# Kernel optimization log

Hardware: AMD Instinct MI355X
Metric: run time of the kernel (lower is better)

## Reference

```python
import jax, jax.numpy as jnp
import numpy as np

TOTAL_WORDS = 10000
EMBED_LEN = 100
SEQ_LEN = 80
BATCH = 2048
UNITS = 1024


def setup_inputs() -> dict:
    key = jax.random.key(0)
    ks = jax.random.split(key, 8)
    inputs = jax.random.randint(ks[0], (BATCH, SEQ_LEN), 0, TOTAL_WORDS)
    s = 0.02
    emb = jax.random.normal(ks[1], (TOTAL_WORDS, EMBED_LEN), jnp.float32) * s
    W0 = jax.random.normal(ks[2], (EMBED_LEN, 4 * UNITS), jnp.float32) * s
    U0 = jax.random.normal(ks[3], (UNITS, 4 * UNITS), jnp.float32) * s
    b0 = jnp.zeros((4 * UNITS,), jnp.float32)
    W1 = jax.random.normal(ks[4], (UNITS, 4 * UNITS), jnp.float32) * s
    U1 = jax.random.normal(ks[5], (UNITS, 4 * UNITS), jnp.float32) * s
    b1 = jnp.zeros((4 * UNITS,), jnp.float32)
    fcW = jax.random.normal(ks[6], (UNITS, 1), jnp.float32) * s
    fcb = jnp.zeros((1,), jnp.float32)
    return {"inputs": inputs, "emb": emb, "W0": W0, "U0": U0, "b0": b0,
            "W1": W1, "U1": U1, "b1": b1, "fcW": fcW, "fcb": fcb}


def _lstm_step(x, h, c, W, U, b):
    # Keras LSTMCell gate order: i, f, g(candidate), o
    z = x @ W + h @ U + b  # [B, 4*units]
    i, f, g, o = jnp.split(z, 4, axis=-1)
    i = jax.nn.sigmoid(i)
    f = jax.nn.sigmoid(f)
    g = jnp.tanh(g)
    o = jax.nn.sigmoid(o)
    c_new = f * c + i * g
    h_new = o * jnp.tanh(c_new)
    return h_new, c_new


def reference(inputs, emb, W0, U0, b0, W1, U1, b1, fcW, fcb):
    x = emb[inputs]                      # [B, T, E]
    xs = jnp.transpose(x, (1, 0, 2))     # [T, B, E] for scan over time
    B = inputs.shape[0]
    U = U0.shape[0]
    init = (jnp.zeros((B, U), x.dtype), jnp.zeros((B, U), x.dtype),
            jnp.zeros((B, U), x.dtype), jnp.zeros((B, U), x.dtype))

    def step(carry, xt):
        h0, c0, h1, c1 = carry
        h0, c0 = _lstm_step(xt, h0, c0, W0, U0, b0)
        h1, c1 = _lstm_step(h0, h1, c1, W1, U1, b1)
        return (h0, c0, h1, c1), None

    (h0, c0, h1, c1), _ = jax.lax.scan(step, init, xs)
    logits = h1 @ fcW + fcb              # [B, 1]
    return jax.nn.sigmoid(logits)
```

## Files before the change

### kernel.cpp

```cpp
#include <hip/hip_runtime.h>

#define DEVI __device__ __forceinline__

typedef __attribute__((ext_vector_type(4))) float f4;
typedef long long i64t;

DEVI unsigned char f2fp8(float x) {
  int p = __builtin_amdgcn_cvt_pk_fp8_f32(x, x, 0, false);
  return (unsigned char)(p & 0xff);
}
DEVI float fp82f(unsigned char b) {
  return __builtin_amdgcn_cvt_f32_fp8((int)b, 0);
}
DEVI float sigmoidf_(float x) { return 1.f / (1.f + __expf(-x)); }
DEVI float tanhf_(float x) {
  float ax = fabsf(x);
  float e = __expf(-2.f * ax);
  float t = (1.f - e) / (1.f + e);
  return x < 0.f ? -t : t;
}

#define GLDS16(g, l) __builtin_amdgcn_global_load_lds( \
    (const __attribute__((address_space(1))) void*)(g), \
    (__attribute__((address_space(3))) void*)(l), 16, 0, 0)

#define SCALE_UP 64.0f
#define SCALE_DN (1.0f / 4096.0f)


__global__ void k_conv_emb(const float* __restrict__ emb, unsigned char* __restrict__ ep) {
  int i = blockIdx.x * 256 + threadIdx.x;
  if (i >= 10000 * 128) return;
  int r = i >> 7, c = i & 127;
  ep[i] = (c < 100) ? f2fp8(emb[r * 100 + c] * SCALE_UP) : (unsigned char)0;
}

DEVI int permn(int n) {
  int g = n >> 10, u = n & 1023;
  return (u >> 5) * 128 + ((u >> 4) & 1) * 64 + g * 16 + (u & 15);
}
DEVI int kswz(int klog, int row) {
  return (klog & ~63) | (((((klog >> 3) & 7) ^ ((row >> 1) & 7))) << 3) | (klog & 7);
}

__global__ void k_conv_w0(const float* __restrict__ W0, const float* __restrict__ U0,
                          unsigned char* __restrict__ WT) {
  int i = blockIdx.x * 256 + threadIdx.x;
  if (i >= 4096 * 1152) return;
  int n = i / 1152, k = i - n * 1152;
  float v;
  if (k < 100) v = W0[k * 4096 + n];
  else if (k < 128) v = 0.f;
  else v = U0[(k - 128) * 4096 + n];
  int np = permn(n);
  WT[(size_t)np * 1152 + kswz(k, np)] = f2fp8(v * SCALE_UP);
}

__global__ void k_conv_w1(const float* __restrict__ W1, const float* __restrict__ U1,
                          unsigned char* __restrict__ WT) {
  int i = blockIdx.x * 256 + threadIdx.x;
  if (i >= 4096 * 2048) return;
  int n = i >> 11, k = i & 2047;
  float v = (k < 1024) ? W1[k * 4096 + n] : U1[(k - 1024) * 4096 + n];
  int np = permn(n);
  WT[(size_t)np * 2048 + kswz(k, np)] = f2fp8(v * SCALE_UP);
}


template<int K1, int KTOT, bool GATHER>
DEVI void lstm_body(int tile, char* smem,
    const unsigned char* __restrict__ src1,
    const unsigned char* __restrict__ src2,
    const int* __restrict__ idx, int t,
    const unsigned char* __restrict__ WT,
    const float* __restrict__ bias,
    float* __restrict__ cbuf,
    unsigned char* __restrict__ hout)
{
  const int tid = threadIdx.x;
  const int bn = tile & 31;
  const int bm = tile >> 5;
  const int m0 = bm * 256;
  const int n0 = bn * 128;

  const int lr = tid >> 2;
  const int c16 = (tid & 3) * 16;
  const int csw = (((tid & 3) ^ ((tid >> 3) & 3))) * 16;

  const unsigned char* g1[2];
  if (GATHER) {
#pragma unroll
    for (int p = 0; p < 2; ++p) {
      int w = idx[(m0 + p * 128 + lr) * 80 + t];
      g1[p] = src1 + (size_t)w * K1 + csw;
    }
  }

  const unsigned char* wbase = WT + (size_t)(n0 + lr) * KTOT + c16;
  const unsigned char* a1b[2];
  const unsigned char* a2b[2];
#pragma unroll
  for (int p = 0; p < 2; ++p) {
    size_t row = (size_t)(m0 + p * 128 + lr);
    a1b[p] = src1 + row * 1024 + c16;
    a2b[p] = src2 + row * 1024 + c16 - K1;
  }

  char* const SAs[3] = {smem, smem + 24576, smem + 49152};

  auto stage = [&](int kb, char* la) {
    char* lb = la + 16384;
    const int kc = kb * 64;
    if (GATHER && kc < K1) {
#pragma unroll
      for (int p = 0; p < 2; ++p)
        GLDS16(g1[p] + kc, la + p * 8192 + tid * 16);
    } else {
#pragma unroll
      for (int p = 0; p < 2; ++p) {
        const unsigned char* g = (!GATHER && kc < K1) ? a1b[p] + kc
                                                      : a2b[p] + kc;
        GLDS16(g, la + p * 8192 + tid * 16);
      }
    }
    GLDS16(wbase + kc, lb + tid * 16);
  };

  const int lane = tid & 63;
  const int wv = tid >> 6;
  const int wm = wv >> 1;
  const int wn = wv & 1;
  const int cl = lane & 15;
  const int qd = lane >> 4;
  const int qh = qd >> 1, qb = qd & 1;
  const int g8s = (cl >> 1) & 7;
  const int ko8_0 = ((0 + qd) ^ g8s) << 3;
  const int ko8_1 = ((4 + qd) ^ g8s) << 3;
  const int g4s = (cl >> 1) & 3;
  const int ko16_0 = ((qh ^ g4s) << 4) + qb * 8;
  const int ko16_1 = (((2 + qh) ^ g4s) << 4) + qb * 8;

  f4 acc[4][4];
  const f4 fz = {0.f, 0.f, 0.f, 0.f};
#pragma unroll
  for (int a = 0; a < 4; ++a)
#pragma unroll
    for (int b = 0; b < 4; ++b) acc[a][b] = fz;

  auto compute = [&](char* la, int koA0, int koA1) {
    char* lb = la + 16384;
#pragma unroll
    for (int kk = 0; kk < 2; ++kk) {
      const int koA = kk ? koA1 : koA0;
      const int koB = kk ? ko8_1 : ko8_0;
      i64t af[4], bfr[4];
#pragma unroll
      for (int mi = 0; mi < 4; ++mi)
        af[mi] = *(const i64t*)(la + (wm * 64 + mi * 16 + cl) * 64 + koA);
#pragma unroll
      for (int j = 0; j < 4; ++j)
        bfr[j] = *(const i64t*)(lb + (wn * 64 + j * 16 + cl) * 64 + koB);
#pragma unroll
      for (int mi = 0; mi < 4; ++mi)
#pragma unroll
        for (int j = 0; j < 4; ++j)
          acc[mi][j] = __builtin_amdgcn_mfma_f32_16x16x32_fp8_fp8(
              af[mi], bfr[j], acc[mi][j], 0, 0, 0);
    }
  };

  stage(0, SAs[0]);
  stage(1, SAs[1]);

  constexpr int NKB = KTOT / 64;
#pragma unroll
  for (int kb = 0; kb < NKB; ++kb) {
    if (kb < NKB - 1)
      asm volatile("s_waitcnt vmcnt(3)" ::: "memory");
    else
      asm volatile("s_waitcnt vmcnt(0)" ::: "memory");
    __builtin_amdgcn_s_barrier();
    if (kb + 2 < NKB) stage(kb + 2, SAs[(kb + 2) % 3]);
    const bool A16 = GATHER && (kb * 64) < K1;
    compute(SAs[kb % 3], A16 ? ko16_0 : ko8_0, A16 ? ko16_1 : ko8_1);
  }

  const int u = bn * 32 + wn * 16 + cl;
  const int uhi = u & ~63;
  const int uc8 = (u >> 3) & 7;
  const int ulo = u & 7;
  const float bi = bias[u];
  const float bff = bias[1024 + u];
  const float bg = bias[2048 + u];
  const float bo = bias[3072 + u];
#pragma unroll
  for (int mi = 0; mi < 4; ++mi) {
    int mbase = m0 + wm * 64 + mi * 16 + qd * 4;
#pragma unroll
    for (int r = 0; r < 4; ++r) {
      int m = mbase + r;
      int fm = (qd * 2 + (r >> 1)) & 7;
      int hcol = uhi | ((uc8 ^ fm) << 3) | ulo;
      float gi = sigmoidf_(acc[mi][0][r] * SCALE_DN + bi);
      float gf = sigmoidf_(acc[mi][1][r] * SCALE_DN + bff);
      float gg = tanhf_(acc[mi][2][r] * SCALE_DN + bg);
      float go = sigmoidf_(acc[mi][3][r] * SCALE_DN + bo);
      size_t coff = (size_t)m * 1024 + u;
      float cn = gf * cbuf[coff] + gi * gg;
      cbuf[coff] = cn;
      hout[(size_t)m * 1024 + hcol] = f2fp8(go * tanhf_(cn) * SCALE_UP);
    }
  }
}

__global__ __launch_bounds__(512, 4) void k_step(
    int mode,
    const unsigned char* embp, const unsigned char* h0in,
    const int* idx, int t,
    const unsigned char* WT0, const float* b0, float* c0, unsigned char* h0out,
    const unsigned char* h0prev, const unsigned char* h1in,
    const unsigned char* WT1, const float* b1, float* c1, unsigned char* h1out)
{
  extern __shared__ char smem[];
  const int blk = blockIdx.x;
  int tile;
  bool isL0;
  if (mode == 1) {
    int hi = (blk >> 8) & 1;
    isL0 = ((blk & 1) ^ hi) != 0;
    tile = hi * 128 + ((blk & 255) >> 1);
  } else {
    tile = blk;
    isL0 = (mode == 0);
  }
  if (isL0)
    lstm_body<128, 1152, true>(tile, smem, embp, h0in, idx, t,
                               WT0, b0, c0, h0out);
  else
    lstm_body<1024, 2048, false>(tile, smem, h0prev, h1in, nullptr, 0,
                                 WT1, b1, c1, h1out);
}


__global__ void k_fc(const unsigned char* __restrict__ h1,
                     const float* __restrict__ fcW, const float* __restrict__ fcb,
                     float* __restrict__ out) {
  int wv = threadIdx.x >> 6;
  int lane = threadIdx.x & 63;
  int row = blockIdx.x * 4 + wv;
  if (row >= 2048) return;
  const unsigned char* hr = h1 + (size_t)row * 1024;
  const int f = (row >> 1) & 7;
  float s = 0.f;
  for (int k = lane; k < 1024; k += 64) {
    int ks = (k & ~63) | ((((k >> 3) & 7) ^ f) << 3) | (k & 7);
    s += fp82f(hr[ks]) * fcW[k];
  }
#pragma unroll
  for (int off = 32; off > 0; off >>= 1) s += __shfl_down(s, off);
  if (lane == 0) out[row] = sigmoidf_(s * (1.0f / SCALE_UP) + fcb[0]);
}


extern "C" void kernel_launch(void* const* d_in, const int* in_sizes, int n_in,
                              void* d_out, int out_size, void* d_ws, size_t ws_size,
                              hipStream_t stream) {
  const int*   idx = (const int*)d_in[0];
  const float* emb = (const float*)d_in[1];
  const float* W0  = (const float*)d_in[2];
  const float* U0  = (const float*)d_in[3];
  const float* b0  = (const float*)d_in[4];
  const float* W1  = (const float*)d_in[5];
  const float* U1  = (const float*)d_in[6];
  const float* b1  = (const float*)d_in[7];
  const float* fcW = (const float*)d_in[8];
  const float* fcb = (const float*)d_in[9];
  float* out = (float*)d_out;

  char* ws = (char*)d_ws;
  unsigned char* embp = (unsigned char*)(ws);
  unsigned char* WT0  = (unsigned char*)(ws + 1280000);
  unsigned char* WT1  = (unsigned char*)(ws + 5998592);
  unsigned char* h0b[2] = {(unsigned char*)(ws + 14387200),
                           (unsigned char*)(ws + 16484352)};
  unsigned char* h1b[2] = {(unsigned char*)(ws + 18581504),
                           (unsigned char*)(ws + 20678656)};
  float* c0 = (float*)(ws + 22775808);
  float* c1 = (float*)(ws + 31164416);

  hipMemsetAsync(ws + 14387200, 0, 25165824, stream);

  k_conv_emb<<<5000, 256, 0, stream>>>(emb, embp);
  k_conv_w0<<<18432, 256, 0, stream>>>(W0, U0, WT0);
  k_conv_w1<<<32768, 256, 0, stream>>>(W1, U1, WT1);

  k_step<<<256, 512, 73728, stream>>>(0, embp, h0b[1], idx, 0,
                                      WT0, b0, c0, h0b[0],
                                      nullptr, nullptr, WT1, b1, c1, nullptr);
  for (int t = 1; t < 80; ++t) {
    k_step<<<512, 512, 73728, stream>>>(1, embp, h0b[(t + 1) & 1], idx, t,
                                        WT0, b0, c0, h0b[t & 1],
                                        h0b[(t - 1) & 1], h1b[t & 1],
                                        WT1, b1, c1, h1b[(t + 1) & 1]);
  }
  k_step<<<256, 512, 73728, stream>>>(2, nullptr, nullptr, nullptr, 0,
                                      WT0, b0, c0, nullptr,
                                      h0b[1], h1b[0], WT1, b1, c1, h1b[1]);

  k_fc<<<512, 256, 0, stream>>>(h1b[1], fcW, fcb, out);
}
```

Baseline: 3.647 ms.

## Shrink LSTM step tiles to 128x128 and run both layers sequentially per block

Changes the step kernel from 512-thread blocks computing 256x128 tiles, with blocks split between layers, to 256-thread blocks computing 128x128 tiles. Each block now runs the layer-0 phase and then the layer-1 phase for the same tile, separated by a block barrier. LDS per block drops from 72KB to 48KB and the launch bounds change to allow different occupancy. The aim is better load balance, since every block does equal work. The cost is less operand reuse per tile and the two layer phases are serialized inside each block rather than running concurrently.

Result: slower. 3.937 ms (+8.0%).

```diff
diff --git a/kernel.cpp b/kernel.cpp
--- a/kernel.cpp
+++ b/kernel.cpp
@@ -68,7 +68,7 @@
 
 
 template<int K1, int KTOT, bool GATHER>
-DEVI void lstm_body(int tile, char* smem,
+DEVI void lstm_phase(int m0, int n0, char* smem,
     const unsigned char* __restrict__ src1,
     const unsigned char* __restrict__ src2,
     const int* __restrict__ idx, int t,
@@ -78,10 +78,6 @@
     unsigned char* __restrict__ hout)
 {
   const int tid = threadIdx.x;
-  const int bn = tile & 31;
-  const int bm = tile >> 5;
-  const int m0 = bm * 256;
-  const int n0 = bn * 128;
 
   const int lr = tid >> 2;
   const int c16 = (tid & 3) * 16;
@@ -91,39 +87,42 @@
   if (GATHER) {
 #pragma unroll
     for (int p = 0; p < 2; ++p) {
-      int w = idx[(m0 + p * 128 + lr) * 80 + t];
+      int w = idx[(m0 + p * 64 + lr) * 80 + t];
       g1[p] = src1 + (size_t)w * K1 + csw;
     }
   }
 
-  const unsigned char* wbase = WT + (size_t)(n0 + lr) * KTOT + c16;
+  const unsigned char* wb[2];
   const unsigned char* a1b[2];
   const unsigned char* a2b[2];
 #pragma unroll
   for (int p = 0; p < 2; ++p) {
-    size_t row = (size_t)(m0 + p * 128 + lr);
+    wb[p]  = WT + (size_t)(n0 + p * 64 + lr) * KTOT + c16;
+    size_t row = (size_t)(m0 + p * 64 + lr);
     a1b[p] = src1 + row * 1024 + c16;
     a2b[p] = src2 + row * 1024 + c16 - K1;
   }
 
-  char* const SAs[3] = {smem, smem + 24576, smem + 49152};
+  char* const SAs[3] = {smem, smem + 16384, smem + 32768};
 
   auto stage = [&](int kb, char* la) {
-    char* lb = la + 16384;
+    char* lb = la + 8192;
     const int kc = kb * 64;
     if (GATHER && kc < K1) {
 #pragma unroll
       for (int p = 0; p < 2; ++p)
-        GLDS16(g1[p] + kc, la + p * 8192 + tid * 16);
+        GLDS16(g1[p] + kc, la + p * 4096 + tid * 16);
     } else {
 #pragma unroll
       for (int p = 0; p < 2; ++p) {
         const unsigned char* g = (!GATHER && kc < K1) ? a1b[p] + kc
                                                       : a2b[p] + kc;
-        GLDS16(g, la + p * 8192 + tid * 16);
+        GLDS16(g, la + p * 4096 + tid * 16);
       }
     }
-    GLDS16(wbase + kc, lb + tid * 16);
+#pragma unroll
+    for (int p = 0; p < 2; ++p)
+      GLDS16(wb[p] + kc, lb + p * 4096 + tid * 16);
   };
 
   const int lane = tid & 63;
@@ -148,7 +147,7 @@
     for (int b = 0; b < 4; ++b) acc[a][b] = fz;
 
   auto compute = [&](char* la, int koA0, int koA1) {
-    char* lb = la + 16384;
+    char* lb = la + 8192;
 #pragma unroll
     for (int kk = 0; kk < 2; ++kk) {
       const int koA = kk ? koA1 : koA0;
@@ -176,7 +175,7 @@
 #pragma unroll
   for (int kb = 0; kb < NKB; ++kb) {
     if (kb < NKB - 1)
-      asm volatile("s_waitcnt vmcnt(3)" ::: "memory");
+      asm volatile("s_waitcnt vmcnt(4)" ::: "memory");
     else
       asm volatile("s_waitcnt vmcnt(0)" ::: "memory");
     __builtin_amdgcn_s_barrier();
@@ -185,7 +184,7 @@
     compute(SAs[kb % 3], A16 ? ko16_0 : ko8_0, A16 ? ko16_1 : ko8_1);
   }
 
-  const int u = bn * 32 + wn * 16 + cl;
+  const int u = n0 / 4 + wn * 16 + cl;
   const int uhi = u & ~63;
   const int uc8 = (u >> 3) & 7;
   const int ulo = u & 7;
@@ -213,7 +212,7 @@
   }
 }
 
-__global__ __launch_bounds__(512, 4) void k_step(
+__global__ __launch_bounds__(256, 2) void k_step(
     int mode,
     const unsigned char* embp, const unsigned char* h0in,
     const int* idx, int t,
@@ -223,22 +222,16 @@
 {
   extern __shared__ char smem[];
   const int blk = blockIdx.x;
-  int tile;
-  bool isL0;
-  if (mode == 1) {
-    int hi = (blk >> 8) & 1;
-    isL0 = ((blk & 1) ^ hi) != 0;
-    tile = hi * 128 + ((blk & 255) >> 1);
-  } else {
-    tile = blk;
-    isL0 = (mode == 0);
-  }
-  if (isL0)
-    lstm_body<128, 1152, true>(tile, smem, embp, h0in, idx, t,
-                               WT0, b0, c0, h0out);
-  else
-    lstm_body<1024, 2048, false>(tile, smem, h0prev, h1in, nullptr, 0,
-                                 WT1, b1, c1, h1out);
+  const int m0 = (blk >> 5) * 128;
+  const int n0 = (blk & 31) * 128;
+  if (mode != 2)
+    lstm_phase<128, 1152, true>(m0, n0, smem, embp, h0in, idx, t,
+                                WT0, b0, c0, h0out);
+  if (mode == 1)
+    __syncthreads();
+  if (mode != 0)
+    lstm_phase<1024, 2048, false>(m0, n0, smem, h0prev, h1in, nullptr, 0,
+                                  WT1, b1, c1, h1out);
 }
 
 
@@ -294,16 +287,16 @@
   k_conv_w0<<<18432, 256, 0, stream>>>(W0, U0, WT0);
   k_conv_w1<<<32768, 256, 0, stream>>>(W1, U1, WT1);
 
-  k_step<<<256, 512, 73728, stream>>>(0, embp, h0b[1], idx, 0,
+  k_step<<<512, 256, 49152, stream>>>(0, embp, h0b[1], idx, 0,
                                       WT0, b0, c0, h0b[0],
                                       nullptr, nullptr, WT1, b1, c1, nullptr);
   for (int t = 1; t < 80; ++t) {
-    k_step<<<512, 512, 73728, stream>>>(1, embp, h0b[(t + 1) & 1], idx, t,
+    k_step<<<512, 256, 49152, stream>>>(1, embp, h0b[(t + 1) & 1], idx, t,
                                         WT0, b0, c0, h0b[t & 1],
                                         h0b[(t - 1) & 1], h1b[t & 1],
                                         WT1, b1, c1, h1b[(t + 1) & 1]);
   }
-  k_step<<<256, 512, 73728, stream>>>(2, nullptr, nullptr, nullptr, 0,
+  k_step<<<512, 256, 49152, stream>>>(2, nullptr, nullptr, nullptr, 0,
                                       WT0, b0, c0, nullptr,
                                       h0b[1], h1b[0], WT1, b1, c1, h1b[1]);
 
```
